# Performance work log

Measured on AMD Instinct MI355X. Metric: run time of the kernel, lower is better.

## Reference

```python
import jax, jax.numpy as jnp
import numpy as np

B, S, E, H, L = 32, 1024, 768, 64, 2  # batch, seq (<=1024 per bias buffer), embed, head hidden, labels
MASKED_BIAS = jnp.float32(-10000.0)


def setup_inputs() -> dict:
    key = jax.random.key(0)
    ks = jax.random.split(key, 12)
    s = 0.02  # init scale
    return {
        "hidden": jax.random.normal(ks[0], (B, S, E), dtype=jnp.float32),
        "attention_mask": jnp.ones((B, S), dtype=jnp.float32),
        # torch nn.Linear weights are [out, in]
        "Wk": jax.random.normal(ks[1], (E, E), dtype=jnp.float32) * s,
        "bk": jnp.zeros((E,), dtype=jnp.float32),
        "Wq": jax.random.normal(ks[2], (E, E), dtype=jnp.float32) * s,
        "bq": jnp.zeros((E,), dtype=jnp.float32),
        "Wv": jax.random.normal(ks[3], (E, E), dtype=jnp.float32) * s,
        "bv": jnp.zeros((E,), dtype=jnp.float32),
        "W1": jax.random.normal(ks[4], (H, E), dtype=jnp.float32) * s,
        "b1": jnp.zeros((H,), dtype=jnp.float32),
        "W2": jax.random.normal(ks[5], (L, H), dtype=jnp.float32) * s,
        "b2": jnp.zeros((L,), dtype=jnp.float32),
    }


def reference(hidden, attention_mask, Wk, bk, Wq, bq, Wv, bv, W1, b1, W2, b2):
    # Single-head causal attention, NO 1/sqrt(d) scaling (faithful to source).
    # Dropout layers run in eval mode -> identity.
    seq = hidden.shape[1]
    q = hidden @ Wq.T + bq            # [B,S,E]
    k = hidden @ Wk.T + bk            # [B,S,E]
    v = hidden @ Wv.T + bv            # [B,S,E] (v_drop is identity in eval)
    w = jnp.einsum('bqe,bke->bqk', q, k)  # [B,S,S]
    causal = jnp.tril(jnp.ones((seq, seq), dtype=bool))  # bias[:, ns-nd:ns, :ns] with nd==ns
    w = jnp.where(causal, w, MASKED_BIAS.astype(w.dtype))
    am = (1.0 - attention_mask)[:, None, :] * -10000.0    # [B,1,S]
    w = jax.nn.softmax(w + am, axis=-1)
    h = jnp.einsum('bqk,bke->bqe', w, v)  # [B,S,E]
    h = jax.nn.relu(h @ W1.T + b1)        # [B,S,64]
    return h @ W2.T + b2                  # [B,S,L]
```

## Files before the change

kernel.cpp:

```cpp
#include <hip/hip_runtime.h>
#include <hip/hip_bf16.h>
#include <cstdio>


typedef _Float16 f16;
typedef f16    f16x8 __attribute__((ext_vector_type(8)));
typedef f16    f16x4 __attribute__((ext_vector_type(4)));
typedef __bf16 bfx8  __attribute__((ext_vector_type(8)));
typedef __bf16 bfx4  __attribute__((ext_vector_type(4)));
typedef float  f32x4 __attribute__((ext_vector_type(4)));

#define MFMA_F16(a,b,c)  __builtin_amdgcn_mfma_f32_16x16x32_f16((a),(b),(c),0,0,0)
#define MFMA_BF16(a,b,c) __builtin_amdgcn_mfma_f32_16x16x32_bf16((a),(b),(c),0,0,0)

static constexpr int LDT2 = 264;

__device__ __forceinline__ void gl_lds16(const void* g, void* l) {
    __builtin_amdgcn_global_load_lds(
        (const __attribute__((address_space(1))) void*)g,
        (__attribute__((address_space(3))) void*)l, 16, 0, 0);
}

#define WAIT_VMCNT(n)                                        \
    do { asm volatile("s_waitcnt vmcnt(" #n ")");            \
         __builtin_amdgcn_sched_barrier(0); } while (0)
#define WAIT_LGKM0()                                         \
    do { asm volatile("s_waitcnt lgkmcnt(0)");               \
         __builtin_amdgcn_sched_barrier(0); } while (0)

__global__ __launch_bounds__(256) void cvt_all(
    const float* __restrict__ hidden,
    const float* __restrict__ Wq, const float* __restrict__ Wk, const float* __restrict__ Wv,
    const float* __restrict__ W1,
    f16* __restrict__ h16, f16* __restrict__ oq, f16* __restrict__ ok, f16* __restrict__ ov,
    __bf16* __restrict__ w1b)
{
    const int bid = blockIdx.x;
    if (bid >= 26304) {
        int base = ((bid - 26304) * 256 + threadIdx.x) * 4;
        f32x4 v = *(const f32x4*)(W1 + base);
        bfx4 o;
        #pragma unroll
        for (int e = 0; e < 4; ++e) o[e] = (__bf16)v[e];
        *(bfx4*)(w1b + base) = o;
        return;
    }
    const float* src;
    f16* dst;
    int base;
    if (bid < 24576) {
        src = hidden; dst = h16;
        base = (bid * 256 + threadIdx.x) * 4;
    } else {
        int wz = (bid - 24576) / 576, wb = (bid - 24576) % 576;
        src = (wz == 0) ? Wq : (wz == 1) ? Wk : Wv;
        dst = (wz == 0) ? oq : (wz == 1) ? ok : ov;
        base = (wb * 256 + threadIdx.x) * 4;
    }
    f32x4 v = *(const f32x4*)(src + base);
    f16x4 o;
    #pragma unroll
    for (int e = 0; e < 4; ++e) o[e] = (f16)v[e];
    *(f16x4*)(dst + base) = o;
}

#define QPHASE(fr0, STAGE_STMT, GATE_STMT)                                        \
    {                                                                             \
        f16x8 afr[2][2];                                                          \
        _Pragma("unroll")                                                         \
        for (int i = 0; i < 2; ++i) {                                             \
            _Pragma("unroll")                                                     \
            for (int kk = 0; kk < 2; ++kk)                                        \
                afr[i][kk] = *(const f16x8*)&SA[kk * 8192 + (wr8 + (fr0) + i) * 512 + lq]; \
        }                                                                         \
        STAGE_STMT;                                                               \
        GATE_STMT;                                                                \
        __builtin_amdgcn_s_barrier();                                             \
        WAIT_LGKM0();                                                             \
        __builtin_amdgcn_s_setprio(1);                                            \
        _Pragma("unroll")                                                         \
        for (int i = 0; i < 2; ++i) {                                             \
            _Pragma("unroll")                                                     \
            for (int jj = 0; jj < 4; ++jj) {                                      \
                acc[(fr0) + i][jj] = MFMA_F16(afr[i][0], bfr[jj][0], acc[(fr0) + i][jj]); \
                acc[(fr0) + i][jj] = MFMA_F16(afr[i][1], bfr[jj][1], acc[(fr0) + i][jj]); \
            }                                                                     \
        }                                                                         \
        __builtin_amdgcn_s_setprio(0);                                            \
        __builtin_amdgcn_s_barrier();                                             \
    }

__global__ __launch_bounds__(512, 2) void qkv_kernel(
    const f16* __restrict__ h16,
    const f16* __restrict__ wq, const f16* __restrict__ wk, const f16* __restrict__ wv,
    const float* __restrict__ bq, const float* __restrict__ bk, const float* __restrict__ bv,
    f16* __restrict__ q16, f16* __restrict__ k16, __bf16* __restrict__ vT)
{
    const int f = blockIdx.x;
    const int xcd = f & 7;
    const int j = f >> 3;
    const int nt = j % 3;
    const int z  = (j / 3) % 3;
    const int mi = j / 9;
    const int mt = xcd + 8 * mi;
    const int m0 = mt * 256, n0 = nt * 256;

    const f16* W = (z == 0) ? wq : (z == 1) ? wk : wv;
    const float* bias = (z == 0) ? bq : (z == 1) ? bk : bv;

    __shared__ alignas(16) f16 S[65536];

    const int t = threadIdx.x, lane = t & 63, wave = t >> 6;
    const int wr = wave >> 2, wc = wave & 3;
    const int wr8 = wr * 8;
    const int quad = lane >> 4, l16 = lane & 15;
    const int lq = quad * 128 + l16 * 8;

    const f16* gA = h16 + (size_t)(m0 + l16) * 768 + quad * 8;
    const f16* gB = W   + (size_t)(n0 + l16) * 768 + quad * 8;
    int gofs[2], lofs[2];
    #pragma unroll
    for (int u = 0; u < 2; ++u) {
        int unit = wave * 2 + u;
        int kk = unit >> 3, c = unit & 7;
        gofs[u] = c * 16 * 768 + kk * 32;
        lofs[u] = kk * 8192 + c * 512;
    }
    auto stage = [&](int kt, int mat, int half) {
        const f16* gp = (mat ? gB : gA) + half * (128 * 768) + kt * 64;
        f16* lp = &S[(kt & 1) * 32768 + mat * 16384 + half * 4096];
        gl_lds16(gp + gofs[0], lp + lofs[0]);
        gl_lds16(gp + gofs[1], lp + lofs[1]);
    };

    f32x4 acc[8][4] = {};

    stage(0, 0, 0); stage(0, 0, 1); stage(0, 1, 0); stage(0, 1, 1);
    stage(1, 1, 0); stage(1, 1, 1);
    WAIT_VMCNT(4);
    __builtin_amdgcn_s_barrier();

    f16x8 bfr[4][2];
    for (int kt = 0; kt < 12; ++kt) {
        const f16* SA = &S[(kt & 1) * 32768];
        const f16* SB = SA + 16384;
        #pragma unroll
        for (int jj = 0; jj < 4; ++jj) {
            #pragma unroll
            for (int kk = 0; kk < 2; ++kk)
                bfr[jj][kk] = *(const f16x8*)&SB[kk * 8192 + (wc * 4 + jj) * 512 + lq];
        }
        QPHASE(0, { if (kt + 1 < 12) stage(kt + 1, 0, 0); }, {});
        QPHASE(2, { if (kt + 1 < 12) stage(kt + 1, 0, 1); }, {});
        QPHASE(4, { if (kt + 2 < 12) stage(kt + 2, 1, 0); }, {});
        QPHASE(6, { if (kt + 2 < 12) stage(kt + 2, 1, 1); },
               {
                   if (kt + 2 < 12)       WAIT_VMCNT(4);
                   else if (kt + 1 < 12)  WAIT_VMCNT(0);
               });
    }

    if (z < 2) {
        f16* out = z ? k16 : q16;
        #pragma unroll
        for (int jj = 0; jj < 4; ++jj) {
            int col = n0 + wc * 64 + jj * 16 + l16;
            float bb = bias[col];
            #pragma unroll
            for (int fi = 0; fi < 8; ++fi) {
                #pragma unroll
                for (int r = 0; r < 4; ++r) {
                    int row = m0 + wr * 128 + fi * 16 + quad * 4 + r;
                    out[(size_t)row * 768 + col] = (f16)(acc[fi][jj][r] + bb);
                }
            }
        }
    } else {
        __bf16* Tb = (__bf16*)S;
        const int halfw = wc >> 1;
        const int bofs = (m0 >> 10) * 768;
        const int s0 = m0 & 1023;
        #pragma unroll
        for (int half = 0; half < 2; ++half) {
            __syncthreads();
            if (halfw == half) {
                #pragma unroll
                for (int jj = 0; jj < 4; ++jj) {
                    int el = (wc & 1) * 64 + jj * 16 + l16;
                    float bb = bias[n0 + half * 128 + el];
                    #pragma unroll
                    for (int fi = 0; fi < 8; ++fi) {
                        #pragma unroll
                        for (int r = 0; r < 4; ++r) {
                            int sl = wr * 128 + fi * 16 + quad * 4 + r;
                            Tb[el * LDT2 + sl] = (__bf16)(acc[fi][jj][r] + bb);
                        }
                    }
                }
            }
            __syncthreads();
            const int ch = (t & 31) * 8;
            const int rbase = t >> 5;
            #pragma unroll
            for (int p = 0; p < 8; ++p) {
                int e = rbase + p * 16;
                bfx8 val = *(const bfx8*)&Tb[e * LDT2 + ch];
                *(bfx8*)&vT[(size_t)(bofs + n0 + half * 128 + e) * 1024 + s0 + ch] = val;
            }
        }
    }
}

__global__ __launch_bounds__(256, 4) void logits_kernel(
    const f16* __restrict__ q16, const f16* __restrict__ k16,
    const float* __restrict__ amask, __bf16* __restrict__ pu, float* __restrict__ psum)
{
    const int f = blockIdx.x;
    const int xcd = f & 7;
    const int j = f >> 3;
    const int b = xcd + 8 * (j / 36);
    const int tile = j % 36;
    int mt = 0, base = 0;
    while (base + mt + 1 <= tile) { base += mt + 1; ++mt; }
    const int nt = tile - base;
    const int m0 = mt * 128, n0 = nt * 128;
    const size_t pb = (size_t)b << 20;
    const size_t qb = (size_t)b * 1024 * 768;

    __shared__ alignas(16) f16 S[2][8192];
    __shared__ float rs[2][128];

    const int t = threadIdx.x, lane = t & 63, wave = t >> 6;
    const int wm = (wave & 1) * 64, wn = (wave >> 1) * 64;
    const int quad = lane >> 4, l16 = lane & 15;

    const f16* gsrc[4];
    int ldst[4];
    #pragma unroll
    for (int u = 0; u < 4; ++u) {
        int c = wave * 4 + u;
        ldst[u] = c * 512;
        const f16* base2 = (c < 8) ? (q16 + qb + (size_t)(m0 + c * 16 + l16) * 768)
                                   : (k16 + qb + (size_t)(n0 + (c - 8) * 16 + l16) * 768);
        gsrc[u] = base2 + quad * 8;
    }

    f32x4 acc[4][4] = {};
    auto stage = [&](int k0, int buf) {
        #pragma unroll
        for (int u = 0; u < 4; ++u)
            gl_lds16(gsrc[u] + k0, &S[buf][ldst[u]]);
    };
    auto compute = [&](int buf) {
        f16x8 af[4], bg[4];
        #pragma unroll
        for (int i = 0; i < 4; ++i) {
            af[i] = *(const f16x8*)&S[buf][(wm / 16 + i) * 512 + quad * 128 + l16 * 8];
            bg[i] = *(const f16x8*)&S[buf][(8 + wn / 16 + i) * 512 + quad * 128 + l16 * 8];
        }
        #pragma unroll
        for (int i = 0; i < 4; ++i)
            #pragma unroll
            for (int jj = 0; jj < 4; ++jj)
                acc[i][jj] = MFMA_F16(af[i], bg[jj], acc[i][jj]);
    };

    stage(0, 0);
    int cur = 0;
    for (int k0 = 32; k0 < 768; k0 += 32) {
        __syncthreads();
        stage(k0, cur ^ 1);
        compute(cur);
        cur ^= 1;
    }
    __syncthreads();
    compute(cur);

    float rp[4][4] = {};
    #pragma unroll
    for (int jj = 0; jj < 4; ++jj) {
        int col = n0 + wn + jj * 16 + l16;
        float am = (1.0f - amask[b * 1024 + col]) * -10000.0f;
        #pragma unroll
        for (int i = 0; i < 4; ++i)
            #pragma unroll
            for (int r = 0; r < 4; ++r) {
                int row = m0 + wm + i * 16 + quad * 4 + r;
                float s = acc[i][jj][r] + am;
                float pval = (col <= row) ? __expf(fminf(s, 80.0f)) : 0.0f;
                pu[pb + (size_t)row * 1024 + col] = (__bf16)pval;
                rp[i][r] += pval;
            }
    }
    #pragma unroll
    for (int i = 0; i < 4; ++i)
        #pragma unroll
        for (int r = 0; r < 4; ++r) {
            float v = rp[i][r];
            v += __shfl_xor(v, 1, 64);
            v += __shfl_xor(v, 2, 64);
            v += __shfl_xor(v, 4, 64);
            v += __shfl_xor(v, 8, 64);
            if (l16 == 0) rs[wn >> 6][wm + i * 16 + quad * 4 + r] = v;
        }
    __syncthreads();
    if (t < 128)
        psum[((size_t)b * 1024 + m0 + t) * 8 + nt] = rs[0][t] + rs[1][t];
}

__global__ __launch_bounds__(256, 4) void pv_kernel(
    const __bf16* __restrict__ pu, const __bf16* __restrict__ vT,
    const float* __restrict__ psum, __bf16* __restrict__ h)
{
    const int f = blockIdx.x;
    const int xcd = f & 7;
    const int j = f >> 3;
    const int b = xcd + 8 * (j / 48);
    const int tile = j % 48;
    const int mt = 7 - tile / 6, nt = tile % 6;
    const int m0 = mt * 128, n0 = nt * 128;
    const size_t pb = (size_t)b << 20;
    const size_t vb = (size_t)b * 768 * 1024;

    __shared__ alignas(16) __bf16 S[2][8192];
    __shared__ float invl[128];

    const int t = threadIdx.x, lane = t & 63, wave = t >> 6;
    const int wm = (wave & 1) * 64, wn = (wave >> 1) * 64;
    const int quad = lane >> 4, l16 = lane & 15;

    if (t < 128) {
        int row = m0 + t;
        int lim = row >> 7;
        const float* pr = &psum[((size_t)b * 1024 + row) * 8];
        float s = 0.f;
        #pragma unroll
        for (int n = 0; n < 8; ++n) s += (n <= lim) ? pr[n] : 0.f;
        invl[t] = 1.0f / s;
    }

    const __bf16* gsrc[4];
    int ldst[4];
    #pragma unroll
    for (int u = 0; u < 4; ++u) {
        int c = wave * 4 + u;
        ldst[u] = c * 512;
        const __bf16* base = (c < 8) ? (pu + pb + (size_t)(m0 + c * 16 + l16) * 1024)
                                     : (vT + vb + (size_t)(n0 + (c - 8) * 16 + l16) * 1024);
        gsrc[u] = base + quad * 8;
    }

    f32x4 acc[4][4] = {};
    auto stage = [&](int k0, int buf) {
        #pragma unroll
        for (int u = 0; u < 4; ++u)
            gl_lds16(gsrc[u] + k0, &S[buf][ldst[u]]);
    };
    auto compute = [&](int buf) {
        bfx8 af[4], bg[4];
        #pragma unroll
        for (int i = 0; i < 4; ++i) {
            af[i] = *(const bfx8*)&S[buf][(wm / 16 + i) * 512 + quad * 128 + l16 * 8];
            bg[i] = *(const bfx8*)&S[buf][(8 + wn / 16 + i) * 512 + quad * 128 + l16 * 8];
        }
        #pragma unroll
        for (int i = 0; i < 4; ++i)
            #pragma unroll
            for (int jj = 0; jj < 4; ++jj)
                acc[i][jj] = MFMA_BF16(af[i], bg[jj], acc[i][jj]);
    };

    const int kend = m0 + 128;
    stage(0, 0);
    int cur = 0;
    for (int k0 = 32; k0 < kend; k0 += 32) {
        __syncthreads();
        stage(k0, cur ^ 1);
        compute(cur);
        cur ^= 1;
    }
    __syncthreads();
    compute(cur);

    #pragma unroll
    for (int jj = 0; jj < 4; ++jj) {
        int col = n0 + wn + jj * 16 + l16;
        #pragma unroll
        for (int i = 0; i < 4; ++i)
            #pragma unroll
            for (int r = 0; r < 4; ++r) {
                int rl = wm + i * 16 + quad * 4 + r;
                h[((size_t)b * 1024 + m0 + rl) * 768 + col] = (__bf16)(acc[i][jj][r] * invl[rl]);
            }
    }
}

__global__ __launch_bounds__(256) void mlp_kernel(
    const __bf16* __restrict__ h, const __bf16* __restrict__ W1b, const float* __restrict__ b1,
    const float* __restrict__ W2, const float* __restrict__ b2, float* __restrict__ out)
{
    const int wave = threadIdx.x >> 6, lane = threadIdx.x & 63;
    const int quad = lane >> 4, l16 = lane & 15;
    const int m0 = blockIdx.x * 64 + wave * 16;

    f32x4 acc[4] = {};
    for (int k0 = 0; k0 < 768; k0 += 32) {
        bfx8 af = *(const bfx8*)&h[(size_t)(m0 + l16) * 768 + k0 + quad * 8];
        #pragma unroll
        for (int jj = 0; jj < 4; ++jj) {
            bfx8 bg = *(const bfx8*)&W1b[(size_t)(jj * 16 + l16) * 768 + k0 + quad * 8];
            acc[jj] = MFMA_BF16(af, bg, acc[jj]);
        }
    }
    float part[4][2] = {};
    #pragma unroll
    for (int jj = 0; jj < 4; ++jj) {
        int c = jj * 16 + l16;
        float bb = b1[c];
        float w20 = W2[c], w21 = W2[64 + c];
        #pragma unroll
        for (int r = 0; r < 4; ++r) {
            float x = fmaxf(acc[jj][r] + bb, 0.f);
            part[r][0] += x * w20;
            part[r][1] += x * w21;
        }
    }
    #pragma unroll
    for (int off = 1; off < 16; off <<= 1)
        #pragma unroll
        for (int r = 0; r < 4; ++r) {
            part[r][0] += __shfl_xor(part[r][0], off, 64);
            part[r][1] += __shfl_xor(part[r][1], off, 64);
        }
    if (l16 == 0) {
        #pragma unroll
        for (int r = 0; r < 4; ++r) {
            int row = m0 + quad * 4 + r;
            out[(size_t)row * 2 + 0] = part[r][0] + b2[0];
            out[(size_t)row * 2 + 1] = part[r][1] + b2[1];
        }
    }
}

extern "C" void kernel_launch(void* const* d_in, const int* in_sizes, int n_in,
                              void* d_out, int out_size, void* d_ws, size_t ws_size,
                              hipStream_t stream)
{
    const float* hidden = (const float*)d_in[0];
    const float* amask  = (const float*)d_in[1];
    const float* Wk = (const float*)d_in[2];
    const float* bk = (const float*)d_in[3];
    const float* Wq = (const float*)d_in[4];
    const float* bq = (const float*)d_in[5];
    const float* Wv = (const float*)d_in[6];
    const float* bv = (const float*)d_in[7];
    const float* W1 = (const float*)d_in[8];
    const float* b1 = (const float*)d_in[9];
    const float* W2 = (const float*)d_in[10];
    const float* b2 = (const float*)d_in[11];
    float* out = (float*)d_out;

    char* ws = (char*)d_ws;
    const size_t MB = 1024 * 1024;
    f16* h16 = (f16*)ws;
    f16* wq16 = (f16*)(ws + 48 * MB);
    f16* wk16 = wq16 + 589824;
    f16* wv16 = wk16 + 589824;
    __bf16* pu  = (__bf16*)ws;
    float*  psum = (float*)(ws + 64 * MB);
    __bf16* w1b = (__bf16*)(ws + 65 * MB);
    f16* q16 = (f16*)(ws + 66 * MB);
    f16* k16 = (f16*)(ws + 114 * MB);
    __bf16* vT = (__bf16*)(ws + 162 * MB);
    __bf16* h  = (__bf16*)(ws + 66 * MB);
    const size_t NEED = 210 * MB;
    if (ws_size < NEED) {
        fprintf(stderr, "[Attn kernel] ws too small: %zu < %zu — skipping launches\n",
                ws_size, NEED);
        return;
    }

    cvt_all<<<24576 + 1728 + 48, 256, 0, stream>>>(
        hidden, Wq, Wk, Wv, W1, h16, wq16, wk16, wv16, w1b);

    qkv_kernel<<<1152, 512, 0, stream>>>(
        h16, wq16, wk16, wv16, bq, bk, bv, q16, k16, vT);
    logits_kernel<<<1152, 256, 0, stream>>>(q16, k16, amask, pu, psum);
    pv_kernel<<<1536, 256, 0, stream>>>(pu, vT, psum, h);
    mlp_kernel<<<512, 256, 0, stream>>>(h, w1b, b1, W2, b2, out);
}
```

Measured before the change: 492.5 us.

## Load GEMM operands directly from global memory and grid-stride the conversion kernel

The logits and PV kernels no longer stage Q/K and P/V tiles through double-buffered LDS with async global-to-LDS loads. Each wave now reads its MFMA fragments straight from global memory, which removes the LDS traffic and barriers but loses sharing of tiles between waves, so each tile is fetched twice from L2. The conversion kernel becomes a grid-stride loop over 2048 blocks, with each thread handling 8 elements. The logits kernel's launch-bounds occupancy hint drops from 4 to 3.

```diff
diff --git a/kernel.cpp b/kernel.cpp
--- a/kernel.cpp
+++ b/kernel.cpp
@@ -35,33 +35,34 @@
     f16* __restrict__ h16, f16* __restrict__ oq, f16* __restrict__ ok, f16* __restrict__ ov,
     __bf16* __restrict__ w1b)
 {
-    const int bid = blockIdx.x;
-    if (bid >= 26304) {
-        int base = ((bid - 26304) * 256 + threadIdx.x) * 4;
-        f32x4 v = *(const f32x4*)(W1 + base);
-        bfx4 o;
-        #pragma unroll
-        for (int e = 0; e < 4; ++e) o[e] = (__bf16)v[e];
-        *(bfx4*)(w1b + base) = o;
-        return;
-    }
-    const float* src;
-    f16* dst;
-    int base;
-    if (bid < 24576) {
-        src = hidden; dst = h16;
-        base = (bid * 256 + threadIdx.x) * 4;
-    } else {
-        int wz = (bid - 24576) / 576, wb = (bid - 24576) % 576;
-        src = (wz == 0) ? Wq : (wz == 1) ? Wk : Wv;
-        dst = (wz == 0) ? oq : (wz == 1) ? ok : ov;
-        base = (wb * 256 + threadIdx.x) * 4;
-    }
-    f32x4 v = *(const f32x4*)(src + base);
-    f16x4 o;
-    #pragma unroll
-    for (int e = 0; e < 4; ++e) o[e] = (f16)v[e];
-    *(f16x4*)(dst + base) = o;
+    const int HID_C = 25165824 / 8;
+    const int W_C   = 589824 / 8;
+    const int W1_C  = 49152 / 8;
+    const int TOT   = HID_C + 3 * W_C + W1_C;
+    for (int c = blockIdx.x * 256 + threadIdx.x; c < TOT; c += 2048 * 256) {
+        const float* src;
+        f16* dst = nullptr;
+        __bf16* dstb = nullptr;
+        int off;
+        if (c < HID_C)                { src = hidden; dst = h16; off = c * 8; }
+        else if (c < HID_C + W_C)     { src = Wq; dst = oq; off = (c - HID_C) * 8; }
+        else if (c < HID_C + 2 * W_C) { src = Wk; dst = ok; off = (c - HID_C - W_C) * 8; }
+        else if (c < HID_C + 3 * W_C) { src = Wv; dst = ov; off = (c - HID_C - 2 * W_C) * 8; }
+        else                          { src = W1; dstb = w1b; off = (c - HID_C - 3 * W_C) * 8; }
+        f32x4 a = *(const f32x4*)(src + off);
+        f32x4 b = *(const f32x4*)(src + off + 4);
+        if (dstb) {
+            bfx8 o;
+            #pragma unroll
+            for (int e = 0; e < 4; ++e) { o[e] = (__bf16)a[e]; o[e + 4] = (__bf16)b[e]; }
+            *(bfx8*)(dstb + off) = o;
+        } else {
+            f16x8 o;
+            #pragma unroll
+            for (int e = 0; e < 4; ++e) { o[e] = (f16)a[e]; o[e + 4] = (f16)b[e]; }
+            *(f16x8*)(dst + off) = o;
+        }
+    }
 }
 
 #define QPHASE(fr0, STAGE_STMT, GATE_STMT)                                        \
@@ -211,7 +212,7 @@
     }
 }
 
-__global__ __launch_bounds__(256, 4) void logits_kernel(
+__global__ __launch_bounds__(256, 3) void logits_kernel(
     const f16* __restrict__ q16, const f16* __restrict__ k16,
     const float* __restrict__ amask, __bf16* __restrict__ pu, float* __restrict__ psum)
 {
@@ -227,54 +228,30 @@
     const size_t pb = (size_t)b << 20;
     const size_t qb = (size_t)b * 1024 * 768;
 
-    __shared__ alignas(16) f16 S[2][8192];
     __shared__ float rs[2][128];
 
     const int t = threadIdx.x, lane = t & 63, wave = t >> 6;
     const int wm = (wave & 1) * 64, wn = (wave >> 1) * 64;
     const int quad = lane >> 4, l16 = lane & 15;
 
-    const f16* gsrc[4];
-    int ldst[4];
-    #pragma unroll
-    for (int u = 0; u < 4; ++u) {
-        int c = wave * 4 + u;
-        ldst[u] = c * 512;
-        const f16* base2 = (c < 8) ? (q16 + qb + (size_t)(m0 + c * 16 + l16) * 768)
-                                   : (k16 + qb + (size_t)(n0 + (c - 8) * 16 + l16) * 768);
-        gsrc[u] = base2 + quad * 8;
-    }
+    const f16* qA = q16 + qb + (size_t)(m0 + wm + l16) * 768 + quad * 8;
+    const f16* kB = k16 + qb + (size_t)(n0 + wn + l16) * 768 + quad * 8;
 
     f32x4 acc[4][4] = {};
-    auto stage = [&](int k0, int buf) {
-        #pragma unroll
-        for (int u = 0; u < 4; ++u)
-            gl_lds16(gsrc[u] + k0, &S[buf][ldst[u]]);
-    };
-    auto compute = [&](int buf) {
+    for (int k0 = 0; k0 < 768; k0 += 32) {
         f16x8 af[4], bg[4];
         #pragma unroll
-        for (int i = 0; i < 4; ++i) {
-            af[i] = *(const f16x8*)&S[buf][(wm / 16 + i) * 512 + quad * 128 + l16 * 8];
-            bg[i] = *(const f16x8*)&S[buf][(8 + wn / 16 + i) * 512 + quad * 128 + l16 * 8];
-        }
+        for (int i = 0; i < 4; ++i)
+            af[i] = *(const f16x8*)(qA + (size_t)i * 16 * 768 + k0);
+        #pragma unroll
+        for (int jj = 0; jj < 4; ++jj)
+            bg[jj] = *(const f16x8*)(kB + (size_t)jj * 16 * 768 + k0);
         #pragma unroll
         for (int i = 0; i < 4; ++i)
             #pragma unroll
             for (int jj = 0; jj < 4; ++jj)
                 acc[i][jj] = MFMA_F16(af[i], bg[jj], acc[i][jj]);
-    };
-
-    stage(0, 0);
-    int cur = 0;
-    for (int k0 = 32; k0 < 768; k0 += 32) {
-        __syncthreads();
-        stage(k0, cur ^ 1);
-        compute(cur);
-        cur ^= 1;
-    }
-    __syncthreads();
-    compute(cur);
+    }
 
     float rp[4][4] = {};
     #pragma unroll
@@ -322,7 +299,6 @@
     const size_t pb = (size_t)b << 20;
     const size_t vb = (size_t)b * 768 * 1024;
 
-    __shared__ alignas(16) __bf16 S[2][8192];
     __shared__ float invl[128];
 
     const int t = threadIdx.x, lane = t & 63, wave = t >> 6;
@@ -338,49 +314,27 @@
         for (int n = 0; n < 8; ++n) s += (n <= lim) ? pr[n] : 0.f;
         invl[t] = 1.0f / s;
     }
-
-    const __bf16* gsrc[4];
-    int ldst[4];
-    #pragma unroll
-    for (int u = 0; u < 4; ++u) {
-        int c = wave * 4 + u;
-        ldst[u] = c * 512;
-        const __bf16* base = (c < 8) ? (pu + pb + (size_t)(m0 + c * 16 + l16) * 1024)
-                                     : (vT + vb + (size_t)(n0 + (c - 8) * 16 + l16) * 1024);
-        gsrc[u] = base + quad * 8;
-    }
-
+    __syncthreads();
+
+    const __bf16* pA = pu + pb + (size_t)(m0 + wm + l16) * 1024 + quad * 8;
+    const __bf16* vB = vT + vb + (size_t)(n0 + wn + l16) * 1024 + quad * 8;
+
+    const int kend = m0 + 128;
     f32x4 acc[4][4] = {};
-    auto stage = [&](int k0, int buf) {
-        #pragma unroll
-        for (int u = 0; u < 4; ++u)
-            gl_lds16(gsrc[u] + k0, &S[buf][ldst[u]]);
-    };
-    auto compute = [&](int buf) {
+    for (int k0 = 0; k0 < kend; k0 += 32) {
         bfx8 af[4], bg[4];
         #pragma unroll
-        for (int i = 0; i < 4; ++i) {
-            af[i] = *(const bfx8*)&S[buf][(wm / 16 + i) * 512 + quad * 128 + l16 * 8];
-            bg[i] = *(const bfx8*)&S[buf][(8 + wn / 16 + i) * 512 + quad * 128 + l16 * 8];
-        }
+        for (int i = 0; i < 4; ++i)
+            af[i] = *(const bfx8*)(pA + (size_t)i * 16 * 1024 + k0);
+        #pragma unroll
+        for (int jj = 0; jj < 4; ++jj)
+            bg[jj] = *(const bfx8*)(vB + (size_t)jj * 16 * 1024 + k0);
         #pragma unroll
         for (int i = 0; i < 4; ++i)
             #pragma unroll
             for (int jj = 0; jj < 4; ++jj)
                 acc[i][jj] = MFMA_BF16(af[i], bg[jj], acc[i][jj]);
-    };
-
-    const int kend = m0 + 128;
-    stage(0, 0);
-    int cur = 0;
-    for (int k0 = 32; k0 < kend; k0 += 32) {
-        __syncthreads();
-        stage(k0, cur ^ 1);
-        compute(cur);
-        cur ^= 1;
-    }
-    __syncthreads();
-    compute(cur);
+    }
 
     #pragma unroll
     for (int jj = 0; jj < 4; ++jj) {
@@ -480,7 +434,7 @@
         return;
     }
 
-    cvt_all<<<24576 + 1728 + 48, 256, 0, stream>>>(
+    cvt_all<<<2048, 256, 0, stream>>>(
         hidden, Wq, Wk, Wv, W1, h16, wq16, wk16, wv16, w1b);
 
     qkv_kernel<<<1152, 512, 0, stream>>>(
```

Result: slower. 588.9 us (+19.6%).

## Stage GEMM epilogues through LDS for coalesced 16-byte stores; grid-stride conversion

Applied to the files above, without the earlier changes.

The q/k, logits and PV kernels now write their accumulator tiles into padded shared memory first. They then read the tiles back so that each thread issues contiguous 16-byte global stores, replacing the scattered 2-byte stores of the MFMA output layout. The fp32-to-half conversion kernel becomes a fixed 2048-block grid-stride loop that handles 8 elements per thread. The new epilogues add barriers and extra LDS traffic, and the qkv kernel's shared buffer grows slightly, which may affect occupancy.

```diff
diff --git a/kernel.cpp b/kernel.cpp
--- a/kernel.cpp
+++ b/kernel.cpp
@@ -14,6 +14,7 @@
 #define MFMA_BF16(a,b,c) __builtin_amdgcn_mfma_f32_16x16x32_bf16((a),(b),(c),0,0,0)
 
 static constexpr int LDT2 = 264;
+static constexpr int LDP  = 136;
 
 __device__ __forceinline__ void gl_lds16(const void* g, void* l) {
     __builtin_amdgcn_global_load_lds(
@@ -35,33 +36,34 @@
     f16* __restrict__ h16, f16* __restrict__ oq, f16* __restrict__ ok, f16* __restrict__ ov,
     __bf16* __restrict__ w1b)
 {
-    const int bid = blockIdx.x;
-    if (bid >= 26304) {
-        int base = ((bid - 26304) * 256 + threadIdx.x) * 4;
-        f32x4 v = *(const f32x4*)(W1 + base);
-        bfx4 o;
-        #pragma unroll
-        for (int e = 0; e < 4; ++e) o[e] = (__bf16)v[e];
-        *(bfx4*)(w1b + base) = o;
-        return;
-    }
-    const float* src;
-    f16* dst;
-    int base;
-    if (bid < 24576) {
-        src = hidden; dst = h16;
-        base = (bid * 256 + threadIdx.x) * 4;
-    } else {
-        int wz = (bid - 24576) / 576, wb = (bid - 24576) % 576;
-        src = (wz == 0) ? Wq : (wz == 1) ? Wk : Wv;
-        dst = (wz == 0) ? oq : (wz == 1) ? ok : ov;
-        base = (wb * 256 + threadIdx.x) * 4;
-    }
-    f32x4 v = *(const f32x4*)(src + base);
-    f16x4 o;
-    #pragma unroll
-    for (int e = 0; e < 4; ++e) o[e] = (f16)v[e];
-    *(f16x4*)(dst + base) = o;
+    const int HID_C = 25165824 / 8;
+    const int W_C   = 589824 / 8;
+    const int W1_C  = 49152 / 8;
+    const int TOT   = HID_C + 3 * W_C + W1_C;
+    for (int c = blockIdx.x * 256 + threadIdx.x; c < TOT; c += 2048 * 256) {
+        const float* src;
+        f16* dst = nullptr;
+        __bf16* dstb = nullptr;
+        int off;
+        if (c < HID_C)                { src = hidden; dst = h16; off = c * 8; }
+        else if (c < HID_C + W_C)     { src = Wq; dst = oq; off = (c - HID_C) * 8; }
+        else if (c < HID_C + 2 * W_C) { src = Wk; dst = ok; off = (c - HID_C - W_C) * 8; }
+        else if (c < HID_C + 3 * W_C) { src = Wv; dst = ov; off = (c - HID_C - 2 * W_C) * 8; }
+        else                          { src = W1; dstb = w1b; off = (c - HID_C - 3 * W_C) * 8; }
+        f32x4 a = *(const f32x4*)(src + off);
+        f32x4 b = *(const f32x4*)(src + off + 4);
+        if (dstb) {
+            bfx8 o;
+            #pragma unroll
+            for (int e = 0; e < 4; ++e) { o[e] = (__bf16)a[e]; o[e + 4] = (__bf16)b[e]; }
+            *(bfx8*)(dstb + off) = o;
+        } else {
+            f16x8 o;
+            #pragma unroll
+            for (int e = 0; e < 4; ++e) { o[e] = (f16)a[e]; o[e + 4] = (f16)b[e]; }
+            *(f16x8*)(dst + off) = o;
+        }
+    }
 }
 
 #define QPHASE(fr0, STAGE_STMT, GATE_STMT)                                        \
@@ -71,7 +73,7 @@
         for (int i = 0; i < 2; ++i) {                                             \
             _Pragma("unroll")                                                     \
             for (int kk = 0; kk < 2; ++kk)                                        \
-                afr[i][kk] = *(const f16x8*)&SA[kk * 8192 + (wr8 + (fr0) + i) * 512 + lq]; \
+                afr[i][kk] = *(const f16x8*)&S[(kt & 1) * 32768 + kk * 8192 + (wr8 + (fr0) + i) * 512 + lq]; \
         }                                                                         \
         STAGE_STMT;                                                               \
         GATE_STMT;                                                                \
@@ -108,7 +110,7 @@
     const f16* W = (z == 0) ? wq : (z == 1) ? wk : wv;
     const float* bias = (z == 0) ? bq : (z == 1) ? bk : bv;
 
-    __shared__ alignas(16) f16 S[65536];
+    __shared__ alignas(16) f16 S[67584];
 
     const int t = threadIdx.x, lane = t & 63, wave = t >> 6;
     const int wr = wave >> 2, wc = wave & 3;
@@ -142,13 +144,11 @@
 
     f16x8 bfr[4][2];
     for (int kt = 0; kt < 12; ++kt) {
-        const f16* SA = &S[(kt & 1) * 32768];
-        const f16* SB = SA + 16384;
         #pragma unroll
         for (int jj = 0; jj < 4; ++jj) {
             #pragma unroll
             for (int kk = 0; kk < 2; ++kk)
-                bfr[jj][kk] = *(const f16x8*)&SB[kk * 8192 + (wc * 4 + jj) * 512 + lq];
+                bfr[jj][kk] = *(const f16x8*)&S[(kt & 1) * 32768 + 16384 + kk * 8192 + (wc * 4 + jj) * 512 + lq];
         }
         QPHASE(0, { if (kt + 1 < 12) stage(kt + 1, 0, 0); }, {});
         QPHASE(2, { if (kt + 1 < 12) stage(kt + 1, 0, 1); }, {});
@@ -162,18 +162,26 @@
 
     if (z < 2) {
         f16* out = z ? k16 : q16;
+        __syncthreads();
         #pragma unroll
         for (int jj = 0; jj < 4; ++jj) {
-            int col = n0 + wc * 64 + jj * 16 + l16;
-            float bb = bias[col];
-            #pragma unroll
-            for (int fi = 0; fi < 8; ++fi) {
+            int cl = wc * 64 + jj * 16 + l16;
+            float bb = bias[n0 + cl];
+            #pragma unroll
+            for (int fi = 0; fi < 8; ++fi)
                 #pragma unroll
-                for (int r = 0; r < 4; ++r) {
-                    int row = m0 + wr * 128 + fi * 16 + quad * 4 + r;
-                    out[(size_t)row * 768 + col] = (f16)(acc[fi][jj][r] + bb);
-                }
-            }
+                for (int r = 0; r < 4; ++r)
+                    S[(wr * 128 + fi * 16 + quad * 4 + r) * LDT2 + cl] =
+                        (f16)(acc[fi][jj][r] + bb);
+        }
+        __syncthreads();
+        const int ch = (t & 31) * 8;
+        const int rb = t >> 5;
+        #pragma unroll
+        for (int p = 0; p < 16; ++p) {
+            int row = rb + p * 16;
+            f16x8 val = *(const f16x8*)&S[row * LDT2 + ch];
+            *(f16x8*)&out[(size_t)(m0 + row) * 768 + n0 + ch] = val;
         }
     } else {
         __bf16* Tb = (__bf16*)S;
@@ -227,7 +235,9 @@
     const size_t pb = (size_t)b << 20;
     const size_t qb = (size_t)b * 1024 * 768;
 
-    __shared__ alignas(16) f16 S[2][8192];
+    __shared__ alignas(16) char smem[34816];
+    f16 (*S)[8192] = (f16 (*)[8192])smem;
+    __bf16* Pb = (__bf16*)smem;
     __shared__ float rs[2][128];
 
     const int t = threadIdx.x, lane = t & 63, wave = t >> 6;
@@ -275,20 +285,22 @@
     }
     __syncthreads();
     compute(cur);
+    __syncthreads();
 
     float rp[4][4] = {};
     #pragma unroll
     for (int jj = 0; jj < 4; ++jj) {
-        int col = n0 + wn + jj * 16 + l16;
+        int cl = wn + jj * 16 + l16;
+        int col = n0 + cl;
         float am = (1.0f - amask[b * 1024 + col]) * -10000.0f;
         #pragma unroll
         for (int i = 0; i < 4; ++i)
             #pragma unroll
             for (int r = 0; r < 4; ++r) {
-                int row = m0 + wm + i * 16 + quad * 4 + r;
+                int rl = wm + i * 16 + quad * 4 + r;
                 float s = acc[i][jj][r] + am;
-                float pval = (col <= row) ? __expf(fminf(s, 80.0f)) : 0.0f;
-                pu[pb + (size_t)row * 1024 + col] = (__bf16)pval;
+                float pval = (col <= m0 + rl) ? __expf(fminf(s, 80.0f)) : 0.0f;
+                Pb[rl * LDP + cl] = (__bf16)pval;
                 rp[i][r] += pval;
             }
     }
@@ -304,6 +316,16 @@
             if (l16 == 0) rs[wn >> 6][wm + i * 16 + quad * 4 + r] = v;
         }
     __syncthreads();
+    {
+        const int ch = (t & 15) * 8;
+        const int rb = t >> 4;
+        #pragma unroll
+        for (int p = 0; p < 8; ++p) {
+            int row = rb + p * 16;
+            bfx8 val = *(const bfx8*)&Pb[row * LDP + ch];
+            *(bfx8*)&pu[pb + (size_t)(m0 + row) * 1024 + n0 + ch] = val;
+        }
+    }
     if (t < 128)
         psum[((size_t)b * 1024 + m0 + t) * 8 + nt] = rs[0][t] + rs[1][t];
 }
@@ -322,7 +344,9 @@
     const size_t pb = (size_t)b << 20;
     const size_t vb = (size_t)b * 768 * 1024;
 
-    __shared__ alignas(16) __bf16 S[2][8192];
+    __shared__ alignas(16) char smem[34816];
+    __bf16 (*S)[8192] = (__bf16 (*)[8192])smem;
+    __bf16* Hb = (__bf16*)smem;
     __shared__ float invl[128];
 
     const int t = threadIdx.x, lane = t & 63, wave = t >> 6;
@@ -381,17 +405,29 @@
     }
     __syncthreads();
     compute(cur);
+    __syncthreads();
 
     #pragma unroll
     for (int jj = 0; jj < 4; ++jj) {
-        int col = n0 + wn + jj * 16 + l16;
+        int cl = wn + jj * 16 + l16;
         #pragma unroll
         for (int i = 0; i < 4; ++i)
             #pragma unroll
             for (int r = 0; r < 4; ++r) {
                 int rl = wm + i * 16 + quad * 4 + r;
-                h[((size_t)b * 1024 + m0 + rl) * 768 + col] = (__bf16)(acc[i][jj][r] * invl[rl]);
+                Hb[rl * LDP + cl] = (__bf16)(acc[i][jj][r] * invl[rl]);
             }
+    }
+    __syncthreads();
+    {
+        const int ch = (t & 15) * 8;
+        const int rb = t >> 4;
+        #pragma unroll
+        for (int p = 0; p < 8; ++p) {
+            int row = rb + p * 16;
+            bfx8 val = *(const bfx8*)&Hb[row * LDP + ch];
+            *(bfx8*)&h[((size_t)b * 1024 + m0 + row) * 768 + n0 + ch] = val;
+        }
     }
 }
 
@@ -480,7 +516,7 @@
         return;
     }
 
-    cvt_all<<<24576 + 1728 + 48, 256, 0, stream>>>(
+    cvt_all<<<2048, 256, 0, stream>>>(
         hidden, Wq, Wk, Wv, W1, h16, wq16, wk16, wv16, w1b);
 
     qkv_kernel<<<1152, 512, 0, stream>>>(
```

New measurement: 487.7 us. Within noise of the previous version (-1.0%).
